# Performance work log

Measured on AMD Instinct MI355X. Metric: run time of the kernel, lower is better.

The kernel has to match this reference:

```python
import jax, jax.numpy as jnp
from jax import lax
import numpy as np

B, N, K = 8, 4096, 64          # clouds, points per cloud, max neighbors
N1, N2 = N // 2, N // 8        # fps ratio 0.5, then 0.25
R1, R2 = 0.2, 0.4              # ball-query radii


def setup_inputs() -> dict:
    key = jax.random.key(0)
    ks = jax.random.split(key, 7)
    def w(k, i, o):
        return jax.random.normal(k, (i, o), jnp.float32) / np.sqrt(i).astype(np.float32)
    return {
        "pos": jax.random.uniform(ks[0], (B, N, 3), jnp.float32),
        "w1a": w(ks[1], 3, 64),    "b1a": jnp.zeros(64, jnp.float32),
        "w1b": w(ks[2], 64, 64),   "b1b": jnp.zeros(64, jnp.float32),
        "w2a": w(ks[3], 67, 128),  "b2a": jnp.zeros(128, jnp.float32),
        "w2b": w(ks[4], 128, 128), "b2b": jnp.zeros(128, jnp.float32),
        "w3a": w(ks[5], 131, 256), "b3a": jnp.zeros(256, jnp.float32),
        "w3b": w(ks[6], 256, 1024),"b3b": jnp.zeros(1024, jnp.float32),
    }


def fps(pos, n_samples):
    # farthest point sampling, deterministic start at index 0. pos: [n, 3]
    d0 = jnp.sum((pos - pos[0]) ** 2, axis=-1)
    def step(mind, _):
        nxt = jnp.argmax(mind)
        d = jnp.sum((pos - pos[nxt]) ** 2, axis=-1)
        return jnp.minimum(mind, d), nxt
    _, idxs = lax.scan(step, d0, None, length=n_samples - 1)
    return jnp.concatenate([jnp.zeros((1,), idxs.dtype), idxs])


def ball_query(centers, pts, r):
    # up to K neighbors within radius r (nearest-first); centers are a subset of pts
    d2 = jnp.sum((centers[:, None, :] - pts[None, :, :]) ** 2, axis=-1)  # [M, n]
    neg = jnp.where(d2 <= r * r, -d2, -jnp.inf)
    vals, nbr = lax.top_k(neg, K)
    return nbr, vals > -jnp.inf  # [M, K] indices, validity mask


def mlp(x, w1, b1, w2, b2, relu_last):
    h = jax.nn.relu(x @ w1 + b1) @ w2 + b2
    return jax.nn.relu(h) if relu_last else h


def masked_max(h, mask):
    # max over neighbor axis; every center has itself as a valid neighbor
    return jnp.max(jnp.where(mask[..., None], h, -jnp.inf), axis=1)


def reference(pos, w1a, b1a, w1b, b1b, w2a, b2a, w2b, b2b, w3a, b3a, w3b, b3b):
    def single(p):  # p: [N, 3]
        # SA1: x is None -> per-edge input is relative position only
        idx1 = fps(p, N1)
        c1 = p[idx1]                                   # [N1, 3]
        nbr1, m1 = ball_query(c1, p, R1)               # [N1, K]
        rel1 = p[nbr1] - c1[:, None, :]                # [N1, K, 3]
        x1 = masked_max(mlp(rel1, w1a, b1a, w1b, b1b, True), m1)   # [N1, 64]
        # SA2: per-edge input is [x_j, pos_j - pos_i]
        idx2 = fps(c1, N2)
        c2 = c1[idx2]                                  # [N2, 3]
        nbr2, m2 = ball_query(c2, c1, R2)              # [N2, K]
        feat2 = jnp.concatenate([x1[nbr2], c1[nbr2] - c2[:, None, :]], axis=-1)  # [N2,K,67]
        x2 = masked_max(mlp(feat2, w2a, b2a, w2b, b2b, True), m2)  # [N2, 128]
        # Global SA: MLP on [x, pos] then global max pool
        g = mlp(jnp.concatenate([x2, c2], axis=-1), w3a, b3a, w3b, b3b, False)   # [N2,1024]
        return jnp.max(g, axis=0)                      # [1024]
    return jax.vmap(single)(pos)                       # [B, 1024]
```

## Files before the change

### kernel.cpp

```cpp
#include <hip/hip_runtime.h>
#include <cstdint>
#include <cstddef>


static constexpr int Bc = 8;
static constexpr int Np = 4096;
static constexpr int Kn = 64;
static constexpr int M1 = 2048;
static constexpr int M2 = 512;
static constexpr int LDX = 132;

#define DEVINL __device__ __forceinline__

DEVINL float d2_exact(float ax, float ay, float az, float bx, float by, float bz) {
    float dx = __fsub_rn(ax, bx);
    float dy = __fsub_rn(ay, by);
    float dz = __fsub_rn(az, bz);
    float xx = __fmul_rn(dx, dx);
    float yy = __fmul_rn(dy, dy);
    float zz = __fmul_rn(dz, dz);
    return __fadd_rn(__fadd_rn(xx, yy), zz);
}

DEVINL unsigned long long wave_max_u64(unsigned long long k) {
    #pragma unroll
    for (int o = 32; o > 0; o >>= 1) {
        unsigned long long other = __shfl_xor(k, o, 64);
        if (other > k) k = other;
    }
    return k;
}

template <int N>
__global__ __launch_bounds__(256)
void fps_kernel(const float* __restrict__ pts, int ns,
                int* __restrict__ idx_out, float* __restrict__ cent) {
    constexpr int PT = N / 256;
    __shared__ float sx_[N], sy_[N], sz_[N];
    __shared__ unsigned long long pbuf[2][4];
    const int b = blockIdx.x;
    const int t = threadIdx.x;
    const int wid = t >> 6;
    const int lane = t & 63;
    const float* base = pts + (size_t)b * N * 3;

    float px[PT], py[PT], pz[PT], mind[PT];
    #pragma unroll
    for (int j = 0; j < PT; ++j) {
        int p = j * 256 + t;
        px[j] = base[p * 3 + 0];
        py[j] = base[p * 3 + 1];
        pz[j] = base[p * 3 + 2];
        sx_[p] = px[j]; sy_[p] = py[j]; sz_[p] = pz[j];
    }
    float x0 = base[0], y0 = base[1], z0 = base[2];
    float bv = -1.0f; int bi = 0;
    #pragma unroll
    for (int j = 0; j < PT; ++j) {
        float d = d2_exact(px[j], py[j], pz[j], x0, y0, z0);
        mind[j] = d;
        if (d > bv) { bv = d; bi = j * 256 + t; }
    }
    unsigned long long key = ((unsigned long long)__float_as_uint(bv) << 32)
                           | (unsigned long long)(0xFFFFFFFFu - (unsigned)bi);
    key = wave_max_u64(key);
    if (lane == 0) pbuf[1][wid] = key;
    if (t == 0) {
        idx_out[(size_t)b * ns] = 0;
        cent[((size_t)b * ns) * 3 + 0] = x0;
        cent[((size_t)b * ns) * 3 + 1] = y0;
        cent[((size_t)b * ns) * 3 + 2] = z0;
    }
    for (int s = 1; s < ns; ++s) {
        __syncthreads();
        unsigned long long k0 = pbuf[s & 1][0];
        unsigned long long k1 = pbuf[s & 1][1];
        unsigned long long k2 = pbuf[s & 1][2];
        unsigned long long k3 = pbuf[s & 1][3];
        unsigned long long ka = k0 > k1 ? k0 : k1;
        unsigned long long kb = k2 > k3 ? k2 : k3;
        unsigned long long km = ka > kb ? ka : kb;
        int idx = (int)(0xFFFFFFFFu - (unsigned)(km & 0xFFFFFFFFull));
        float cx = sx_[idx], cy = sy_[idx], cz = sz_[idx];
        if (t == 0) {
            idx_out[(size_t)b * ns + s] = idx;
            cent[((size_t)b * ns + s) * 3 + 0] = cx;
            cent[((size_t)b * ns + s) * 3 + 1] = cy;
            cent[((size_t)b * ns + s) * 3 + 2] = cz;
        }
        bv = -1.0f; bi = 0;
        #pragma unroll
        for (int j = 0; j < PT; ++j) {
            float d = d2_exact(px[j], py[j], pz[j], cx, cy, cz);
            float m = fminf(mind[j], d);
            mind[j] = m;
            if (m > bv) { bv = m; bi = j * 256 + t; }
        }
        key = ((unsigned long long)__float_as_uint(bv) << 32)
            | (unsigned long long)(0xFFFFFFFFu - (unsigned)bi);
        key = wave_max_u64(key);
        if (lane == 0) pbuf[(s + 1) & 1][wid] = key;
    }
}

template <int NPT>
__global__ __launch_bounds__(256)
void bq_kernel(const float* __restrict__ pts, const float* __restrict__ ctr,
               int mshift, float r2, int* __restrict__ nbr) {
    constexpr int CH = NPT / 64;
    const int lane = threadIdx.x & 63;
    int w = __builtin_amdgcn_readfirstlane((int)(blockIdx.x * 4 + (threadIdx.x >> 6)));
    const int b = w >> mshift;
    const float* pb = pts + (size_t)b * NPT * 3;
    const float* cp = ctr + (size_t)w * 3;
    float cx = cp[0], cy = cp[1], cz = cp[2];
    const unsigned r2b = __float_as_uint(r2);

    unsigned ub[CH];
    int cnt = 0;
    #pragma unroll
    for (int j = 0; j < CH; ++j) {
        int p = j * 64 + lane;
        float d = d2_exact(pb[p * 3 + 0], pb[p * 3 + 1], pb[p * 3 + 2], cx, cy, cz);
        ub[j] = __float_as_uint(d);
        cnt += __popcll(__ballot(ub[j] <= r2b));
    }
    int* out = nbr + (size_t)w * Kn;
    const unsigned long long lml = (1ull << lane) - 1ull;

    if (cnt <= Kn) {
        int basep = 0;
        #pragma unroll
        for (int j = 0; j < CH; ++j) {
            bool v = ub[j] <= r2b;
            unsigned long long mk = __ballot(v);
            if (v) out[basep + __popcll(mk & lml)] = j * 64 + lane;
            basep += __popcll(mk);
        }
        if (lane >= cnt) out[lane] = -1;
    } else {
        unsigned lo = 0, hi = r2b;
        while (lo < hi) {
            unsigned mid = lo + ((hi - lo) >> 1);
            int c = 0;
            #pragma unroll
            for (int j = 0; j < CH; ++j) c += __popcll(__ballot(ub[j] <= mid));
            if (c >= Kn) hi = mid; else lo = mid + 1;
        }
        const unsigned tt = lo;
        int cntLess = 0;
        #pragma unroll
        for (int j = 0; j < CH; ++j) cntLess += __popcll(__ballot(ub[j] < tt));
        const int quota = Kn - cntLess;
        int baseLt = 0, eqseen = 0;
        #pragma unroll
        for (int j = 0; j < CH; ++j) {
            bool lt = ub[j] < tt;
            bool eq = ub[j] == tt;
            unsigned long long mlt = __ballot(lt);
            unsigned long long meq = __ballot(eq);
            if (lt) out[baseLt + __popcll(mlt & lml)] = j * 64 + lane;
            if (eq) {
                int rr = eqseen + __popcll(meq & lml);
                if (rr < quota) out[cntLess + rr] = j * 64 + lane;
            }
            baseLt += __popcll(mlt);
            eqseen += __popcll(meq);
        }
    }
}

__global__ __launch_bounds__(256)
void mlp1_kernel(const float* __restrict__ pos, const float* __restrict__ c1,
                 const int* __restrict__ nbr, const float* __restrict__ w1aT,
                 const float* __restrict__ w1bT, const float* __restrict__ b1b,
                 float* __restrict__ x1) {
    const int lane = threadIdx.x & 63;
    int w = __builtin_amdgcn_readfirstlane((int)(blockIdx.x * 4 + (threadIdx.x >> 6)));
    const int b = w >> 11;
    const int ii = nbr[(size_t)w * Kn + lane];
    const bool valid = ii >= 0;
    const int i2 = valid ? ii : 0;
    const float* pp = pos + ((size_t)b * Np + i2) * 3;
    const float* cc = c1 + (size_t)w * 3;
    float rx = pp[0] - cc[0], ry = pp[1] - cc[1], rz = pp[2] - cc[2];
    float h1[64];
    #pragma unroll
    for (int h = 0; h < 64; ++h) {
        float4 wv = ((const float4*)w1aT)[h];
        float a = fmaf(rx, wv.x, fmaf(ry, wv.y, fmaf(rz, wv.z, wv.w)));
        h1[h] = fmaxf(a, 0.0f);
    }
    float* orow = x1 + (size_t)w * 64;
    for (int c4 = 0; c4 < 16; ++c4) {
        float v4[4];
        #pragma unroll
        for (int cq = 0; cq < 4; ++cq) {
            int c = c4 * 4 + cq;
            float acc = b1b[c];
            const float4* wr = (const float4*)(w1bT + (size_t)c * 64);
            #pragma unroll
            for (int q = 0; q < 16; ++q) {
                float4 wv = wr[q];
                acc = fmaf(h1[4 * q + 0], wv.x, acc);
                acc = fmaf(h1[4 * q + 1], wv.y, acc);
                acc = fmaf(h1[4 * q + 2], wv.z, acc);
                acc = fmaf(h1[4 * q + 3], wv.w, acc);
            }
            float v = fmaxf(acc, 0.0f);
            v = valid ? v : -__builtin_inff();
            #pragma unroll
            for (int o = 32; o > 0; o >>= 1) v = fmaxf(v, __shfl_xor(v, o, 64));
            v4[cq] = v;
        }
        if (lane == 0)
            ((float4*)orow)[c4] = make_float4(v4[0], v4[1], v4[2], v4[3]);
    }
}

__global__ __launch_bounds__(256)
void mlp2_kernel(const float* __restrict__ x1, const float* __restrict__ c1,
                 const float* __restrict__ c2, const int* __restrict__ nbr2,
                 const float* __restrict__ w2aT, const float* __restrict__ w2bT,
                 const float* __restrict__ b2b, float* __restrict__ X) {
    const int lane = threadIdx.x & 63;
    int w = __builtin_amdgcn_readfirstlane((int)(blockIdx.x * 4 + (threadIdx.x >> 6)));
    const int b = w >> 9;
    const int ii = nbr2[(size_t)w * Kn + lane];
    const bool valid = ii >= 0;
    const int i2 = valid ? ii : 0;

    float x[68];
    const float4* xr = (const float4*)(x1 + ((size_t)b * M1 + i2) * 64);
    #pragma unroll
    for (int q = 0; q < 16; ++q) {
        float4 v = xr[q];
        x[4 * q + 0] = v.x; x[4 * q + 1] = v.y;
        x[4 * q + 2] = v.z; x[4 * q + 3] = v.w;
    }
    const float* cc = c2 + (size_t)w * 3;
    const float* cp = c1 + ((size_t)b * M1 + i2) * 3;
    x[64] = cp[0] - cc[0];
    x[65] = cp[1] - cc[1];
    x[66] = cp[2] - cc[2];
    x[67] = 0.0f;

    float h1[128];
    #pragma unroll
    for (int h = 0; h < 128; ++h) {
        const float4* r4 = (const float4*)(w2aT + (size_t)h * 80);
        float acc = 0.0f;
        #pragma unroll
        for (int q = 0; q < 16; ++q) {
            float4 wv = r4[q];
            acc = fmaf(x[4 * q + 0], wv.x, acc);
            acc = fmaf(x[4 * q + 1], wv.y, acc);
            acc = fmaf(x[4 * q + 2], wv.z, acc);
            acc = fmaf(x[4 * q + 3], wv.w, acc);
        }
        float4 tl = r4[16];
        acc = fmaf(x[64], tl.x, acc);
        acc = fmaf(x[65], tl.y, acc);
        acc = fmaf(x[66], tl.z, acc);
        acc += tl.w;
        h1[h] = fmaxf(acc, 0.0f);
    }
    float* orow = X + (size_t)w * LDX;
    for (int c4 = 0; c4 < 32; ++c4) {
        float v4[4];
        #pragma unroll
        for (int cq = 0; cq < 4; ++cq) {
            int c = c4 * 4 + cq;
            float acc = b2b[c];
            const float4* wr = (const float4*)(w2bT + (size_t)c * 128);
            #pragma unroll
            for (int q = 0; q < 32; ++q) {
                float4 wv = wr[q];
                acc = fmaf(h1[4 * q + 0], wv.x, acc);
                acc = fmaf(h1[4 * q + 1], wv.y, acc);
                acc = fmaf(h1[4 * q + 2], wv.z, acc);
                acc = fmaf(h1[4 * q + 3], wv.w, acc);
            }
            float v = fmaxf(acc, 0.0f);
            v = valid ? v : -__builtin_inff();
            #pragma unroll
            for (int o = 32; o > 0; o >>= 1) v = fmaxf(v, __shfl_xor(v, o, 64));
            v4[cq] = v;
        }
        if (lane == 0) {
            orow[c4 * 4 + 0] = v4[0]; orow[c4 * 4 + 1] = v4[1];
            orow[c4 * 4 + 2] = v4[2]; orow[c4 * 4 + 3] = v4[3];
        }
    }
}

__global__ __launch_bounds__(256)
void writec2_kernel(const float* __restrict__ c2, float* __restrict__ X) {
    int i = blockIdx.x * 256 + threadIdx.x;
    if (i < Bc * M2 * 3) {
        int w = i / 3, d = i - w * 3;
        X[(size_t)w * LDX + 128 + d] = c2[i];
    }
}

__global__ __launch_bounds__(256)
void gemm1_kernel(const float* __restrict__ X, const float* __restrict__ w3a,
                  const float* __restrict__ b3a, float* __restrict__ H) {
    const int r = blockIdx.x;
    const int c = threadIdx.x;
    const float* xr = X + (size_t)r * LDX;
    float acc = b3a[c];
    for (int i = 0; i < 131; ++i)
        acc = fmaf(xr[i], w3a[(size_t)i * 256 + c], acc);
    H[(size_t)r * 256 + c] = fmaxf(acc, 0.0f);
}

__global__ __launch_bounds__(256)
void gemm2_kernel(const float* __restrict__ H, const float* __restrict__ w3b,
                  float* __restrict__ part) {
    __shared__ float As[32][33];
    __shared__ float Bs[32][64];
    __shared__ float red[8][64];
    const int bidx = blockIdx.x;
    const int nt = bidx & 15;
    const int mt = (bidx >> 4) & 15;
    const int b = bidx >> 8;
    const int row0 = b * M2 + mt * 32;
    const int col0 = nt * 64;
    const int t = threadIdx.x;
    const int rg = t >> 5, cg = t & 31;

    float acc[4][2] = {{0.f, 0.f}, {0.f, 0.f}, {0.f, 0.f}, {0.f, 0.f}};
    for (int k0 = 0; k0 < 256; k0 += 32) {
        #pragma unroll
        for (int q = 0; q < 4; ++q) {
            int id = t + q * 256;
            As[id >> 5][id & 31] = H[(size_t)(row0 + (id >> 5)) * 256 + k0 + (id & 31)];
        }
        #pragma unroll
        for (int q = 0; q < 8; ++q) {
            int id = t + q * 256;
            Bs[id >> 6][id & 63] = w3b[(size_t)(k0 + (id >> 6)) * 1024 + col0 + (id & 63)];
        }
        __syncthreads();
        #pragma unroll
        for (int kk = 0; kk < 32; ++kk) {
            float b0 = Bs[kk][cg * 2 + 0];
            float b1 = Bs[kk][cg * 2 + 1];
            #pragma unroll
            for (int j = 0; j < 4; ++j) {
                float a = As[rg * 4 + j][kk];
                acc[j][0] = fmaf(a, b0, acc[j][0]);
                acc[j][1] = fmaf(a, b1, acc[j][1]);
            }
        }
        __syncthreads();
    }
    float m0 = fmaxf(fmaxf(acc[0][0], acc[1][0]), fmaxf(acc[2][0], acc[3][0]));
    float m1 = fmaxf(fmaxf(acc[0][1], acc[1][1]), fmaxf(acc[2][1], acc[3][1]));
    red[rg][cg * 2 + 0] = m0;
    red[rg][cg * 2 + 1] = m1;
    __syncthreads();
    if (t < 64) {
        float v = red[0][t];
        #pragma unroll
        for (int q = 1; q < 8; ++q) v = fmaxf(v, red[q][t]);
        part[((size_t)b * 16 + mt) * 1024 + col0 + t] = v;
    }
}

__global__ __launch_bounds__(256)
void rmax_kernel(const float* __restrict__ part, const float* __restrict__ b3b,
                 float* __restrict__ out) {
    int i = blockIdx.x * 256 + threadIdx.x;
    int b = i >> 10, c = i & 1023;
    float v = -__builtin_inff();
    #pragma unroll
    for (int tt = 0; tt < 16; ++tt)
        v = fmaxf(v, part[((size_t)b * 16 + tt) * 1024 + c]);
    out[i] = v + b3b[c];
}

__global__ __launch_bounds__(256)
void prep_kernel(const float* __restrict__ w1a, const float* __restrict__ b1a,
                 const float* __restrict__ w1b, const float* __restrict__ w2a,
                 const float* __restrict__ b2a, const float* __restrict__ w2b,
                 float* __restrict__ w1aT, float* __restrict__ w1bT,
                 float* __restrict__ w2aT, float* __restrict__ w2bT) {
    int i = blockIdx.x * 256 + threadIdx.x;
    if (i < 64 * 4) {
        int h = i >> 2, d = i & 3;
        w1aT[i] = (d < 3) ? w1a[d * 64 + h] : b1a[h];
    }
    if (i < 64 * 64) {
        int c = i >> 6, h = i & 63;
        w1bT[i] = w1b[h * 64 + c];
    }
    if (i < 128 * 80) {
        int h = i / 80, d = i - h * 80;
        w2aT[i] = (d < 67) ? w2a[d * 128 + h] : ((d == 67) ? b2a[h] : 0.0f);
    }
    {
        int c = i >> 7, h = i & 127;
        w2bT[i] = w2b[h * 128 + c];
    }
}

extern "C" void kernel_launch(void* const* d_in, const int* in_sizes, int n_in,
                              void* d_out, int out_size, void* d_ws, size_t ws_size,
                              hipStream_t stream) {
    const float* pos = (const float*)d_in[0];
    const float* w1a = (const float*)d_in[1];
    const float* b1a = (const float*)d_in[2];
    const float* w1b = (const float*)d_in[3];
    const float* b1b = (const float*)d_in[4];
    const float* w2a = (const float*)d_in[5];
    const float* b2a = (const float*)d_in[6];
    const float* w2b = (const float*)d_in[7];
    const float* b2b = (const float*)d_in[8];
    const float* w3a = (const float*)d_in[9];
    const float* b3a = (const float*)d_in[10];
    const float* w3b = (const float*)d_in[11];
    const float* b3b = (const float*)d_in[12];
    float* out = (float*)d_out;

    char* ws = (char*)d_ws;
    size_t off = 0;
    auto alloc = [&](size_t bytes) -> char* {
        char* p = ws + off;
        off += (bytes + 255) & ~(size_t)255;
        return p;
    };
    float* c1   = (float*)alloc(sizeof(float) * Bc * M1 * 3);
    float* c2   = (float*)alloc(sizeof(float) * Bc * M2 * 3);
    int*   idx1 = (int*)alloc(sizeof(int) * Bc * M1);
    int*   idx2 = (int*)alloc(sizeof(int) * Bc * M2);
    int*   nbr1 = (int*)alloc(sizeof(int) * Bc * M1 * Kn);
    int*   nbr2 = (int*)alloc(sizeof(int) * Bc * M2 * Kn);
    float* x1   = (float*)alloc(sizeof(float) * Bc * M1 * 64);
    float* X    = (float*)alloc(sizeof(float) * Bc * M2 * LDX);
    float* H    = (float*)alloc(sizeof(float) * Bc * M2 * 256);
    float* part = (float*)alloc(sizeof(float) * Bc * 16 * 1024);
    float* w1aT = (float*)alloc(sizeof(float) * 64 * 4);
    float* w1bT = (float*)alloc(sizeof(float) * 64 * 64);
    float* w2aT = (float*)alloc(sizeof(float) * 128 * 80);
    float* w2bT = (float*)alloc(sizeof(float) * 128 * 128);

    prep_kernel<<<dim3(64), dim3(256), 0, stream>>>(w1a, b1a, w1b, w2a, b2a, w2b,
                                                    w1aT, w1bT, w2aT, w2bT);
    fps_kernel<Np><<<dim3(Bc), dim3(256), 0, stream>>>(pos, M1, idx1, c1);
    bq_kernel<Np><<<dim3(Bc * M1 / 4), dim3(256), 0, stream>>>(
        pos, c1, 11, (float)(0.2 * 0.2), nbr1);
    mlp1_kernel<<<dim3(Bc * M1 / 4), dim3(256), 0, stream>>>(
        pos, c1, nbr1, w1aT, w1bT, b1b, x1);
    fps_kernel<M1><<<dim3(Bc), dim3(256), 0, stream>>>(c1, M2, idx2, c2);
    bq_kernel<M1><<<dim3(Bc * M2 / 4), dim3(256), 0, stream>>>(
        c1, c2, 9, (float)(0.4 * 0.4), nbr2);
    mlp2_kernel<<<dim3(Bc * M2 / 4), dim3(256), 0, stream>>>(
        x1, c1, c2, nbr2, w2aT, w2bT, b2b, X);
    writec2_kernel<<<dim3(48), dim3(256), 0, stream>>>(c2, X);
    gemm1_kernel<<<dim3(Bc * M2), dim3(256), 0, stream>>>(X, w3a, b3a, H);
    gemm2_kernel<<<dim3(Bc * 16 * 16), dim3(256), 0, stream>>>(H, w3b, part);
    rmax_kernel<<<dim3(32), dim3(256), 0, stream>>>(part, b3b, out);
}
```

Before: 2.787 ms.

## Use DPP wave max and 512-thread blocks in farthest point sampling

Replaces the shuffle-based 64-bit wave argmax in the FPS kernel with a DPP row-shift/row-broadcast reduction whose result lands in lane 63. It also doubles the FPS block size to 512 threads (8 waves), halving points per thread, and reads the eight per-wave partials as 128-bit loads. This targets the serial per-step latency of the FPS loop, which runs on only 8 blocks. In exchange, the cross-wave barrier now spans more waves, and the DPP bound_ctrl and row masks must be exactly right for correctness.

```diff
diff --git a/kernel.cpp b/kernel.cpp
--- a/kernel.cpp
+++ b/kernel.cpp
@@ -22,22 +22,34 @@
     return __fadd_rn(__fadd_rn(xx, yy), zz);
 }
 
-DEVINL unsigned long long wave_max_u64(unsigned long long k) {
-    #pragma unroll
-    for (int o = 32; o > 0; o >>= 1) {
-        unsigned long long other = __shfl_xor(k, o, 64);
-        if (other > k) k = other;
-    }
+template <int CTRL, int RM, int BM>
+DEVINL unsigned long long dpp_max_step(unsigned long long k) {
+    unsigned lo = (unsigned)k, hi = (unsigned)(k >> 32);
+    unsigned slo = (unsigned)__builtin_amdgcn_update_dpp(0, (int)lo, CTRL, RM, BM, true);
+    unsigned shi = (unsigned)__builtin_amdgcn_update_dpp(0, (int)hi, CTRL, RM, BM, true);
+    unsigned long long s = ((unsigned long long)shi << 32) | (unsigned long long)slo;
+    return s > k ? s : k;
+}
+
+DEVINL unsigned long long wave_max_u64_dpp(unsigned long long k) {
+    k = dpp_max_step<0x111, 0xf, 0xf>(k);
+    k = dpp_max_step<0x112, 0xf, 0xf>(k);
+    k = dpp_max_step<0x114, 0xf, 0xf>(k);
+    k = dpp_max_step<0x118, 0xf, 0xf>(k);
+    k = dpp_max_step<0x142, 0xa, 0xf>(k);
+    k = dpp_max_step<0x143, 0xc, 0xf>(k);
     return k;
 }
 
 template <int N>
-__global__ __launch_bounds__(256)
+__global__ __launch_bounds__(512)
 void fps_kernel(const float* __restrict__ pts, int ns,
                 int* __restrict__ idx_out, float* __restrict__ cent) {
-    constexpr int PT = N / 256;
+    constexpr int NT = 512;
+    constexpr int NW = NT / 64;
+    constexpr int PT = N / NT;
     __shared__ float sx_[N], sy_[N], sz_[N];
-    __shared__ unsigned long long pbuf[2][4];
+    __shared__ alignas(16) unsigned long long pbuf[2][NW];
     const int b = blockIdx.x;
     const int t = threadIdx.x;
     const int wid = t >> 6;
@@ -47,7 +59,7 @@
     float px[PT], py[PT], pz[PT], mind[PT];
     #pragma unroll
     for (int j = 0; j < PT; ++j) {
-        int p = j * 256 + t;
+        int p = j * NT + t;
         px[j] = base[p * 3 + 0];
         py[j] = base[p * 3 + 1];
         pz[j] = base[p * 3 + 2];
@@ -59,12 +71,12 @@
     for (int j = 0; j < PT; ++j) {
         float d = d2_exact(px[j], py[j], pz[j], x0, y0, z0);
         mind[j] = d;
-        if (d > bv) { bv = d; bi = j * 256 + t; }
+        if (d > bv) { bv = d; bi = j * NT + t; }
     }
     unsigned long long key = ((unsigned long long)__float_as_uint(bv) << 32)
                            | (unsigned long long)(0xFFFFFFFFu - (unsigned)bi);
-    key = wave_max_u64(key);
-    if (lane == 0) pbuf[1][wid] = key;
+    key = wave_max_u64_dpp(key);
+    if (lane == 63) pbuf[1][wid] = key;
     if (t == 0) {
         idx_out[(size_t)b * ns] = 0;
         cent[((size_t)b * ns) * 3 + 0] = x0;
@@ -73,12 +85,14 @@
     }
     for (int s = 1; s < ns; ++s) {
         __syncthreads();
-        unsigned long long k0 = pbuf[s & 1][0];
-        unsigned long long k1 = pbuf[s & 1][1];
-        unsigned long long k2 = pbuf[s & 1][2];
-        unsigned long long k3 = pbuf[s & 1][3];
-        unsigned long long ka = k0 > k1 ? k0 : k1;
-        unsigned long long kb = k2 > k3 ? k2 : k3;
+        const ulonglong2* pb2 = (const ulonglong2*)pbuf[s & 1];
+        ulonglong2 q0 = pb2[0], q1 = pb2[1], q2 = pb2[2], q3 = pb2[3];
+        unsigned long long a0 = q0.x > q0.y ? q0.x : q0.y;
+        unsigned long long a1 = q1.x > q1.y ? q1.x : q1.y;
+        unsigned long long a2 = q2.x > q2.y ? q2.x : q2.y;
+        unsigned long long a3 = q3.x > q3.y ? q3.x : q3.y;
+        unsigned long long ka = a0 > a1 ? a0 : a1;
+        unsigned long long kb = a2 > a3 ? a2 : a3;
         unsigned long long km = ka > kb ? ka : kb;
         int idx = (int)(0xFFFFFFFFu - (unsigned)(km & 0xFFFFFFFFull));
         float cx = sx_[idx], cy = sy_[idx], cz = sz_[idx];
@@ -94,12 +108,12 @@
             float d = d2_exact(px[j], py[j], pz[j], cx, cy, cz);
             float m = fminf(mind[j], d);
             mind[j] = m;
-            if (m > bv) { bv = m; bi = j * 256 + t; }
+            if (m > bv) { bv = m; bi = j * NT + t; }
         }
         key = ((unsigned long long)__float_as_uint(bv) << 32)
             | (unsigned long long)(0xFFFFFFFFu - (unsigned)bi);
-        key = wave_max_u64(key);
-        if (lane == 0) pbuf[(s + 1) & 1][wid] = key;
+        key = wave_max_u64_dpp(key);
+        if (lane == 63) pbuf[(s + 1) & 1][wid] = key;
     }
 }
 
@@ -448,12 +462,12 @@
 
     prep_kernel<<<dim3(64), dim3(256), 0, stream>>>(w1a, b1a, w1b, w2a, b2a, w2b,
                                                     w1aT, w1bT, w2aT, w2bT);
-    fps_kernel<Np><<<dim3(Bc), dim3(256), 0, stream>>>(pos, M1, idx1, c1);
+    fps_kernel<Np><<<dim3(Bc), dim3(512), 0, stream>>>(pos, M1, idx1, c1);
     bq_kernel<Np><<<dim3(Bc * M1 / 4), dim3(256), 0, stream>>>(
         pos, c1, 11, (float)(0.2 * 0.2), nbr1);
     mlp1_kernel<<<dim3(Bc * M1 / 4), dim3(256), 0, stream>>>(
         pos, c1, nbr1, w1aT, w1bT, b1b, x1);
-    fps_kernel<M1><<<dim3(Bc), dim3(256), 0, stream>>>(c1, M2, idx2, c2);
+    fps_kernel<M1><<<dim3(Bc), dim3(512), 0, stream>>>(c1, M2, idx2, c2);
     bq_kernel<M1><<<dim3(Bc * M2 / 4), dim3(256), 0, stream>>>(
         c1, c2, 9, (float)(0.4 * 0.4), nbr2);
     mlp2_kernel<<<dim3(Bc * M2 / 4), dim3(256), 0, stream>>>(
```

Result: faster. 2.630 ms (-5.6%).
